# Kernel tuning notes

Hardware: AMD Instinct MI355X
Metric: run time of the kernel (lower is better)

The kernel has to match this reference:

```python
import jax, jax.numpy as jnp
import numpy as np

B, L, P, NH = 16384, 64, 2, 128
T = L // P          # number of patches (GRU steps)
NOUT = 1 << P       # softmax over 2**p possible patches


def setup_inputs() -> dict:
    key = jax.random.key(0)
    ks = jax.random.split(key, 10)
    s_in = 1.0 / np.sqrt(NH)
    x = jax.random.randint(ks[0], (B, L, 1), 0, 2).astype(jnp.float32)
    return {
        "x": x,
        # GRU params, torch layout: gates ordered (r, z, n)
        "w_ih": jax.random.normal(ks[1], (3 * NH, P), jnp.float32) * s_in,
        "w_hh": jax.random.normal(ks[2], (3 * NH, NH), jnp.float32) * s_in,
        "b_ih": jax.random.normal(ks[3], (3 * NH,), jnp.float32) * s_in,
        "b_hh": jax.random.normal(ks[4], (3 * NH,), jnp.float32) * s_in,
        # MLP head: Linear(Nh,Nh) -> ReLU -> Linear(Nh, 2**p) -> Softmax
        "w1": jax.random.normal(ks[5], (NH, NH), jnp.float32) * s_in,
        "b1": jax.random.normal(ks[6], (NH,), jnp.float32) * s_in,
        "w2": jax.random.normal(ks[7], (NOUT, NH), jnp.float32) * s_in,
        "b2": jax.random.normal(ks[8], (NOUT,), jnp.float32) * s_in,
    }


def _gru_mlp_logp(x, w_ih, w_hh, b_ih, b_hh, w1, b1, w2, b2):
    b = x.shape[0]
    patches = x.reshape(b, T, P)                       # Patch1D.forward
    # shift right by one patch (teacher forcing input), first step is zeros
    data = jnp.concatenate([jnp.zeros((b, 1, P), x.dtype), patches[:, :-1]], axis=1)
    # precompute all input-side gate projections: [B,T,3*Nh]
    xi = jnp.einsum('btp,gp->btg', data, w_ih) + b_ih

    def step(h, xi_t):
        gi_r, gi_z, gi_n = jnp.split(xi_t, 3, axis=-1)
        gh = h @ w_hh.T + b_hh
        gh_r, gh_z, gh_n = jnp.split(gh, 3, axis=-1)
        r = jax.nn.sigmoid(gi_r + gh_r)
        z = jax.nn.sigmoid(gi_z + gh_z)
        n = jnp.tanh(gi_n + r * gh_n)
        h_new = (1.0 - z) * n + z * h
        return h_new, h_new

    h0 = jnp.zeros((b, NH), x.dtype)
    _, hs = jax.lax.scan(step, h0, jnp.swapaxes(xi, 0, 1))  # [T,B,Nh]
    hs = jnp.swapaxes(hs, 0, 1)                              # [B,T,Nh]

    hid = jax.nn.relu(hs @ w1.T + b1)
    probs = jax.nn.softmax(hid @ w2.T + b2, axis=-1)         # [B,T,2**p]

    # genpatch2onehot: binary-encode each patch, little-endian (bit i -> 2**i)
    weights = (1 << jnp.arange(P)).astype(jnp.float32)
    idx = jnp.sum(patches * weights, axis=-1).astype(jnp.int32)  # [B,T]
    total = jnp.take_along_axis(probs, idx[..., None], axis=-1)[..., 0]
    return jnp.sum(jnp.log(total), axis=1)                   # [B]


def reference(x, w_ih, w_hh, b_ih, b_hh, w1, b1, w2, b2):
    return _gru_mlp_logp(x, w_ih, w_hh, b_ih, b_hh, w1, b1, w2, b2)
```

## Files before the change

kernel.cpp:

```cpp
#include <hip/hip_runtime.h>
#include <hip/hip_bf16.h>


#define NSTEP 32
#define BT    32
#define BLK   512

using s8v = __attribute__((ext_vector_type(8))) short;
using f4v = __attribute__((ext_vector_type(4))) float;

#define L2E 1.4426950408889634f
#define LN2 0.6931471805599453f

__device__ __forceinline__ unsigned short f2bf(float f) {
  __hip_bfloat16 h = __float2bfloat16(f);
  return __builtin_bit_cast(unsigned short, h);
}
__device__ __forceinline__ unsigned pkbf2(float a, float b) {
  return (unsigned)f2bf(a) | ((unsigned)f2bf(b) << 16);
}
__device__ __forceinline__ s8v pack8s(float sc, float4 u, float4 v) {
  s8v a;
  a[0]=(short)f2bf(sc*u.x); a[1]=(short)f2bf(sc*u.y); a[2]=(short)f2bf(sc*u.z); a[3]=(short)f2bf(sc*u.w);
  a[4]=(short)f2bf(sc*v.x); a[5]=(short)f2bf(sc*v.y); a[6]=(short)f2bf(sc*v.z); a[7]=(short)f2bf(sc*v.w);
  return a;
}
__device__ __forceinline__ f4v mfma16(s8v a, s8v b, f4v c) {
  return __builtin_amdgcn_mfma_f32_16x16x32_bf16(a, b, c, 0, 0, 0);
}
__device__ __forceinline__ float sigm2(float x) {
  return __builtin_amdgcn_rcpf(1.f + __builtin_amdgcn_exp2f(-x));
}
__device__ __forceinline__ float tanh2(float x) {
  return __builtin_fmaf(2.f, __builtin_amdgcn_rcpf(1.f + __builtin_amdgcn_exp2f(-x)), -1.f);
}

__global__ __launch_bounds__(BLK, 4) void prnn_kernel(
    const float* __restrict__ x, const float* __restrict__ w_ih,
    const float* __restrict__ w_hh, const float* __restrict__ b_ih,
    const float* __restrict__ b_hh, const float* __restrict__ w1,
    const float* __restrict__ b1, const float* __restrict__ w2,
    const float* __restrict__ b2, float* __restrict__ out) {

  __shared__ __align__(16) unsigned char lds_h[2][8192];
  __shared__ __align__(16) unsigned char lds_hid[2][8192];
  __shared__ __align__(16) unsigned char lds_wA1[8*4*64*16];
  __shared__ __align__(16) unsigned char lds_w2f[4*64*16];
  __shared__ __align__(16) float lds_xrz[64*4*4];
  __shared__ __align__(16) float lds_xn[32*4*4];
  __shared__ __align__(16) float lds_bb[256];
  __shared__ __align__(16) float lds_b2[4];
  __shared__ unsigned lds_idx[32*8];
  __shared__ float lds_lp[8][32];

  const int tid = threadIdx.x;
  const int bbase = blockIdx.x * BT;
  const int lane = tid & 63;
  const int lg = lane >> 4, ln = lane & 15;
  const int w = __builtin_amdgcn_readfirstlane(tid >> 6);

  if (tid < 256) {
    int b = tid >> 3, ch = tid & 7;
    const float* xp = x + (size_t)(bbase + b) * 64 + ch * 8;
    float4 v0 = *(const float4*)xp, v1 = *(const float4*)(xp + 4);
    unsigned pk = ((v0.x!=0.f?1u:0u) | (v0.y!=0.f?2u:0u))
               | (((v0.z!=0.f?1u:0u) | (v0.w!=0.f?2u:0u)) << 8)
               | (((v1.x!=0.f?1u:0u) | (v1.y!=0.f?2u:0u)) << 16)
               | (((v1.z!=0.f?1u:0u) | (v1.w!=0.f?2u:0u)) << 24);
    lds_idx[b*8 + ch] = pk;
  }
  if (tid < 256) {
    int j = tid;
    float base = b_ih[j] + b_hh[j];
    float wa = w_ih[2*j], wb = w_ih[2*j+1];
    int q = j >> 2, e = j & 3;
    #pragma unroll
    for (int v = 0; v < 4; ++v)
      lds_xrz[(q*4+v)*4 + e] = L2E * (base + ((v&1) ? wa : 0.f) + ((v&2) ? wb : 0.f));
  }
  if (tid < 128) {
    int j2 = 256 + tid;
    float bn = b_ih[j2];
    float wan = w_ih[2*j2], wbn = w_ih[2*j2+1];
    int qn = tid >> 2, en = tid & 3;
    #pragma unroll
    for (int v = 0; v < 4; ++v)
      lds_xn[(qn*4+v)*4 + en] = (2.f*L2E) * (bn + ((v&1) ? wan : 0.f) + ((v&2) ? wbn : 0.f));
  }
  if (tid < 128) lds_bb[tid] = (2.f*L2E) * b_hh[256 + tid];
  else if (tid < 256) lds_bb[tid] = b1[tid - 128];
  if (tid < 4) lds_b2[tid] = b2[tid];
  #pragma unroll
  for (int it = 0; it < 4; ++it) {
    int i = tid + it * BLK;
    int mt = i >> 8, ks = (i >> 6) & 3, l = i & 63;
    const float* src = w1 + (16*mt + (l & 15)) * 128 + ks*32 + (l >> 4)*8;
    *(s8v*)(lds_wA1 + ((mt*4 + ks)*64 + l)*16) = pack8s(1.f, *(const float4*)src, *(const float4*)(src+4));
  }
  if (tid < 256) {
    int ks = tid >> 6, l = tid & 63;
    s8v fr;
    #pragma unroll
    for (int e = 0; e < 8; ++e) fr[e] = (short)0;
    if ((l & 15) < 4) {
      const float* src = w2 + (l & 15) * 128 + ks*32 + (l >> 4)*8;
      fr = pack8s(1.f, *(const float4*)src, *(const float4*)(src + 4));
    }
    *(s8v*)(lds_w2f + (ks*64 + l)*16) = fr;
  }

  s8v Ar[4], Az[4], An[4];
  {
    const int row = 16*w + ln;
    #pragma unroll
    for (int ks = 0; ks < 4; ++ks) {
      const float* s0 = w_hh + row*128 + ks*32 + lg*8;
      Ar[ks] = pack8s(L2E, *(const float4*)s0, *(const float4*)(s0 + 4));
      const float* s1 = s0 + 128*128;
      Az[ks] = pack8s(L2E, *(const float4*)s1, *(const float4*)(s1 + 4));
      const float* s2 = s0 + 256*128;
      An[ks] = pack8s(2.f*L2E, *(const float4*)s2, *(const float4*)(s2 + 4));
    }
  }
  const int q = 4*w + lg;

  __syncthreads();

  unsigned pk0a=0, pk0b=0, pk1a=0, pk1b=0;
  #pragma unroll
  for (int w8 = 0; w8 < 4; ++w8) {
    unsigned u = lds_idx[ln*8 + w8];
    pk0a |= (((u&3u) | ((u>>6)&0xCu) | ((u>>12)&0x30u) | ((u>>18)&0xC0u)) << (8*w8));
    unsigned u2 = lds_idx[(16+ln)*8 + w8];
    pk1a |= (((u2&3u) | ((u2>>6)&0xCu) | ((u2>>12)&0x30u) | ((u2>>18)&0xC0u)) << (8*w8));
  }
  #pragma unroll
  for (int w8 = 4; w8 < 8; ++w8) {
    unsigned u = lds_idx[ln*8 + w8];
    pk0b |= (((u&3u) | ((u>>6)&0xCu) | ((u>>12)&0x30u) | ((u>>18)&0xC0u)) << (8*(w8-4)));
    unsigned u2 = lds_idx[(16+ln)*8 + w8];
    pk1b |= (((u2&3u) | ((u2>>6)&0xCu) | ((u2>>12)&0x30u) | ((u2>>18)&0xC0u)) << (8*(w8-4)));
  }

  const unsigned wroff = (unsigned)((((w>>1)*128) + 16*(2*(w&1) + (lg>>1)) + ln)*16 + 8*(lg&1));

  s8v Bf[4][2];
  #pragma unroll
  for (int ks = 0; ks < 4; ++ks)
    #pragma unroll
    for (int nt = 0; nt < 2; ++nt)
      #pragma unroll
      for (int e = 0; e < 8; ++e) Bf[ks][nt][e] = (short)0;
  f4v hfr[2];
  hfr[0][0]=0.f; hfr[0][1]=0.f; hfr[0][2]=0.f; hfr[0][3]=0.f;
  hfr[1] = hfr[0];
  float lp0 = 0.f, lp1 = 0.f;
  int pv0 = 0, pv1 = 0;

  auto do_p5 = [&](int u, int uslot) {
    const int ua = u & 7;
    const bool d0 = (w == ua), d1 = (w == (ua ^ 4));
    if (d0 | d1) {
      const int ntx = d1 ? 1 : 0;
      f4v la;
      if (lg == 0) la = *(const f4v*)lds_b2;
      else { la[0]=0.f; la[1]=0.f; la[2]=0.f; la[3]=0.f; }
      #pragma unroll
      for (int ks = 0; ks < 4; ++ks) {
        const s8v W2f = *(const s8v*)(lds_w2f + (ks*64 + lane)*16);
        const s8v Bh  = *(const s8v*)(&lds_hid[uslot][((ks*2 + ntx)*64 + lane)*16]);
        la = mfma16(W2f, Bh, la);
      }
      if (lg == 0) {
        const unsigned hsel = ntx ? ((u & 16) ? pk1b : pk1a) : ((u & 16) ? pk0b : pk0a);
        const int ic = (int)((hsel >> ((2*u) & 31)) & 3);
        float l0=la[0], l1=la[1], l2=la[2], l3=la[3];
        float m = fmaxf(fmaxf(l0, l1), fmaxf(l2, l3));
        float s = __builtin_amdgcn_exp2f((l0-m)*L2E) + __builtin_amdgcn_exp2f((l1-m)*L2E)
                + __builtin_amdgcn_exp2f((l2-m)*L2E) + __builtin_amdgcn_exp2f((l3-m)*L2E);
        float sel = (ic == 0) ? l0 : (ic == 1) ? l1 : (ic == 2) ? l2 : l3;
        float v = (sel - m) - __builtin_amdgcn_logf(s) * LN2;
        if (ntx) lp1 += v; else lp0 += v;
      }
    }
  };

  for (int tb = 0; tb < NSTEP; tb += 8) {
    #pragma unroll
    for (int k = 0; k < 8; ++k) {
      const int t = tb + k;
      const int slot = t & 1;
      #pragma unroll
      for (int nt = 0; nt < 2; ++nt) {
        const int var = nt ? pv1 : pv0;
        f4v aR = *(const f4v*)&lds_xrz[(q*4 + var)*4];
        f4v aZ = *(const f4v*)&lds_xrz[((q+32)*4 + var)*4];
        f4v aN = *(const f4v*)&lds_bb[q*4];
        #pragma unroll
        for (int ks = 0; ks < 4; ++ks) {
          aR = mfma16(Ar[ks], Bf[ks][nt], aR);
          aZ = mfma16(Az[ks], Bf[ks][nt], aZ);
          aN = mfma16(An[ks], Bf[ks][nt], aN);
        }
        const f4v xnv = *(const f4v*)&lds_xn[(q*4 + var)*4];
        f4v hn;
        #pragma unroll
        for (int r = 0; r < 4; ++r) {
          float R  = sigm2(aR[r]);
          float Z  = sigm2(aZ[r]);
          float Ng = tanh2(__builtin_fmaf(R, aN[r], xnv[r]));
          hn[r] = __builtin_fmaf(Z, hfr[nt][r] - Ng, Ng);
        }
        hfr[nt] = hn;
        uint2 wv;
        wv.x = pkbf2(hn[0], hn[1]);
        wv.y = pkbf2(hn[2], hn[3]);
        *(uint2*)(&lds_h[slot][wroff + (unsigned)(nt*1024)]) = wv;
      }
      __syncthreads();
      if (t > 0) do_p5(t - 1, slot ^ 1);
      #pragma unroll
      for (int ks = 0; ks < 4; ++ks)
        #pragma unroll
        for (int nt = 0; nt < 2; ++nt)
          Bf[ks][nt] = *(const s8v*)(&lds_h[slot][((ks*2 + nt)*64 + lane)*16]);
      const f4v b1i = *(const f4v*)&lds_bb[128 + q*4];
      f4v hc0 = b1i, hc1 = b1i;
      #pragma unroll
      for (int ks = 0; ks < 4; ++ks) {
        const s8v wf = *(const s8v*)(lds_wA1 + ((w*4 + ks)*64 + lane)*16);
        hc0 = mfma16(wf, Bf[ks][0], hc0);
        hc1 = mfma16(wf, Bf[ks][1], hc1);
      }
      {
        uint2 wv;
        wv.x = pkbf2(fmaxf(hc0[0],0.f), fmaxf(hc0[1],0.f));
        wv.y = pkbf2(fmaxf(hc0[2],0.f), fmaxf(hc0[3],0.f));
        *(uint2*)(&lds_hid[slot][wroff]) = wv;
        wv.x = pkbf2(fmaxf(hc1[0],0.f), fmaxf(hc1[1],0.f));
        wv.y = pkbf2(fmaxf(hc1[2],0.f), fmaxf(hc1[3],0.f));
        *(uint2*)(&lds_hid[slot][wroff + 1024u]) = wv;
      }
      {
        const unsigned g0 = (t & 16) ? pk0b : pk0a;
        const unsigned g1 = (t & 16) ? pk1b : pk1a;
        const int sh = (2*t) & 31;
        pv0 = (int)((g0 >> sh) & 3);
        pv1 = (int)((g1 >> sh) & 3);
      }
    }
  }

  __syncthreads();
  do_p5(NSTEP - 1, (NSTEP - 1) & 1);

  if (lg == 0) { lds_lp[w][ln] = lp0; lds_lp[w][16 + ln] = lp1; }
  __syncthreads();
  if (tid < 32) {
    float s = 0.f;
    #pragma unroll
    for (int ww = 0; ww < 8; ++ww) s += lds_lp[ww][tid];
    out[bbase + tid] = s;
  }
}

extern "C" void kernel_launch(void* const* d_in, const int* in_sizes, int n_in,
                              void* d_out, int out_size, void* d_ws, size_t ws_size,
                              hipStream_t stream) {
  const float* x    = (const float*)d_in[0];
  const float* w_ih = (const float*)d_in[1];
  const float* w_hh = (const float*)d_in[2];
  const float* b_ih = (const float*)d_in[3];
  const float* b_hh = (const float*)d_in[4];
  const float* w1   = (const float*)d_in[5];
  const float* b1   = (const float*)d_in[6];
  const float* w2   = (const float*)d_in[7];
  const float* b2   = (const float*)d_in[8];
  float* out = (float*)d_out;
  int B = in_sizes[0] / 64;
  int grid = B / BT;
  prnn_kernel<<<grid, BLK, 0, stream>>>(x, w_ih, w_hh, b_ih, b_hh, w1, b1, w2, b2, out);
}
```

Baseline: 111.2 us.

## Halve batch tile per block and preconvert MLP weights in a prep kernel

Each block now handles 16 sequences instead of 32, which doubles the grid and removes the second n-tile of work per wave. The w1/w2 bf16 fragments are built once by a separate prep kernel into workspace and read from global/L2 instead of being repacked into LDS per block. The head's softmax step is now done in-step behind an extra barrier rather than deferred, and LDS double-buffering is dropped. The trade is more barriers per step and global loads of weight fragments inside the recurrence loop, in exchange for more blocks and less LDS per block.

```diff
diff --git a/kernel.cpp b/kernel.cpp
--- a/kernel.cpp
+++ b/kernel.cpp
@@ -3,7 +3,7 @@
 
 
 #define NSTEP 32
-#define BT    32
+#define BT    16
 #define BLK   512
 
 using s8v = __attribute__((ext_vector_type(8))) short;
@@ -35,23 +35,42 @@
   return __builtin_fmaf(2.f, __builtin_amdgcn_rcpf(1.f + __builtin_amdgcn_exp2f(-x)), -1.f);
 }
 
+__global__ void prep_kernel(const float* __restrict__ w1, const float* __restrict__ w2,
+                            unsigned char* __restrict__ ws) {
+  const int task = blockIdx.x;
+  const int l = threadIdx.x;
+  if (task < 32) {
+    const int mt = task >> 2, ks = task & 3;
+    const float* src = w1 + (16*mt + (l & 15)) * 128 + ks*32 + (l >> 4)*8;
+    *(s8v*)(ws + (task*64 + l)*16) = pack8s(1.f, *(const float4*)src, *(const float4*)(src + 4));
+  } else {
+    const int ks = task - 32;
+    s8v fr;
+    #pragma unroll
+    for (int e = 0; e < 8; ++e) fr[e] = (short)0;
+    if ((l & 15) < 4) {
+      const float* src = w2 + (l & 15) * 128 + ks*32 + (l >> 4)*8;
+      fr = pack8s(1.f, *(const float4*)src, *(const float4*)(src + 4));
+    }
+    *(s8v*)(ws + 32768 + (ks*64 + l)*16) = fr;
+  }
+}
+
 __global__ __launch_bounds__(BLK, 4) void prnn_kernel(
     const float* __restrict__ x, const float* __restrict__ w_ih,
     const float* __restrict__ w_hh, const float* __restrict__ b_ih,
-    const float* __restrict__ b_hh, const float* __restrict__ w1,
-    const float* __restrict__ b1, const float* __restrict__ w2,
-    const float* __restrict__ b2, float* __restrict__ out) {
-
-  __shared__ __align__(16) unsigned char lds_h[2][8192];
-  __shared__ __align__(16) unsigned char lds_hid[2][8192];
-  __shared__ __align__(16) unsigned char lds_wA1[8*4*64*16];
-  __shared__ __align__(16) unsigned char lds_w2f[4*64*16];
+    const float* __restrict__ b_hh, const float* __restrict__ b1,
+    const float* __restrict__ b2, const unsigned char* __restrict__ ws,
+    float* __restrict__ out) {
+
+  __shared__ __align__(16) unsigned char lds_h[4*64*16];
+  __shared__ __align__(16) unsigned char lds_hid[4*64*16];
   __shared__ __align__(16) float lds_xrz[64*4*4];
   __shared__ __align__(16) float lds_xn[32*4*4];
   __shared__ __align__(16) float lds_bb[256];
   __shared__ __align__(16) float lds_b2[4];
-  __shared__ unsigned lds_idx[32*8];
-  __shared__ float lds_lp[8][32];
+  __shared__ unsigned lds_idx[16*8];
+  __shared__ float lds_lp[8][16];
 
   const int tid = threadIdx.x;
   const int bbase = blockIdx.x * BT;
@@ -59,7 +78,7 @@
   const int lg = lane >> 4, ln = lane & 15;
   const int w = __builtin_amdgcn_readfirstlane(tid >> 6);
 
-  if (tid < 256) {
+  if (tid < 128) {
     int b = tid >> 3, ch = tid & 7;
     const float* xp = x + (size_t)(bbase + b) * 64 + ch * 8;
     float4 v0 = *(const float4*)xp, v1 = *(const float4*)(xp + 4);
@@ -73,10 +92,10 @@
     int j = tid;
     float base = b_ih[j] + b_hh[j];
     float wa = w_ih[2*j], wb = w_ih[2*j+1];
-    int q = j >> 2, e = j & 3;
+    int qq = j >> 2, e = j & 3;
     #pragma unroll
     for (int v = 0; v < 4; ++v)
-      lds_xrz[(q*4+v)*4 + e] = L2E * (base + ((v&1) ? wa : 0.f) + ((v&2) ? wb : 0.f));
+      lds_xrz[(qq*4+v)*4 + e] = L2E * (base + ((v&1) ? wa : 0.f) + ((v&2) ? wb : 0.f));
   }
   if (tid < 128) {
     int j2 = 256 + tid;
@@ -90,24 +109,6 @@
   if (tid < 128) lds_bb[tid] = (2.f*L2E) * b_hh[256 + tid];
   else if (tid < 256) lds_bb[tid] = b1[tid - 128];
   if (tid < 4) lds_b2[tid] = b2[tid];
-  #pragma unroll
-  for (int it = 0; it < 4; ++it) {
-    int i = tid + it * BLK;
-    int mt = i >> 8, ks = (i >> 6) & 3, l = i & 63;
-    const float* src = w1 + (16*mt + (l & 15)) * 128 + ks*32 + (l >> 4)*8;
-    *(s8v*)(lds_wA1 + ((mt*4 + ks)*64 + l)*16) = pack8s(1.f, *(const float4*)src, *(const float4*)(src+4));
-  }
-  if (tid < 256) {
-    int ks = tid >> 6, l = tid & 63;
-    s8v fr;
-    #pragma unroll
-    for (int e = 0; e < 8; ++e) fr[e] = (short)0;
-    if ((l & 15) < 4) {
-      const float* src = w2 + (l & 15) * 128 + ks*32 + (l >> 4)*8;
-      fr = pack8s(1.f, *(const float4*)src, *(const float4*)(src + 4));
-    }
-    *(s8v*)(lds_w2f + (ks*64 + l)*16) = fr;
-  }
 
   s8v Ar[4], Az[4], An[4];
   {
@@ -123,84 +124,47 @@
     }
   }
   const int q = 4*w + lg;
+  const s8v* __restrict__ wsf = (const s8v*)ws;
 
   __syncthreads();
 
-  unsigned pk0a=0, pk0b=0, pk1a=0, pk1b=0;
+  unsigned pk0a = 0, pk0b = 0;
   #pragma unroll
   for (int w8 = 0; w8 < 4; ++w8) {
     unsigned u = lds_idx[ln*8 + w8];
     pk0a |= (((u&3u) | ((u>>6)&0xCu) | ((u>>12)&0x30u) | ((u>>18)&0xC0u)) << (8*w8));
-    unsigned u2 = lds_idx[(16+ln)*8 + w8];
-    pk1a |= (((u2&3u) | ((u2>>6)&0xCu) | ((u2>>12)&0x30u) | ((u2>>18)&0xC0u)) << (8*w8));
-  }
-  #pragma unroll
-  for (int w8 = 4; w8 < 8; ++w8) {
-    unsigned u = lds_idx[ln*8 + w8];
-    pk0b |= (((u&3u) | ((u>>6)&0xCu) | ((u>>12)&0x30u) | ((u>>18)&0xC0u)) << (8*(w8-4)));
-    unsigned u2 = lds_idx[(16+ln)*8 + w8];
-    pk1b |= (((u2&3u) | ((u2>>6)&0xCu) | ((u2>>12)&0x30u) | ((u2>>18)&0xC0u)) << (8*(w8-4)));
-  }
-
-  const unsigned wroff = (unsigned)((((w>>1)*128) + 16*(2*(w&1) + (lg>>1)) + ln)*16 + 8*(lg&1));
-
-  s8v Bf[4][2];
+    unsigned u2 = lds_idx[ln*8 + 4 + w8];
+    pk0b |= (((u2&3u) | ((u2>>6)&0xCu) | ((u2>>12)&0x30u) | ((u2>>18)&0xC0u)) << (8*w8));
+  }
+
+  const unsigned wroff =
+      (unsigned)((((w>>1)*64 + 16*(2*(w&1) + (lg>>1)) + ln)*16) + 8*(lg&1));
+
+  s8v Bf[4];
   #pragma unroll
   for (int ks = 0; ks < 4; ++ks)
     #pragma unroll
-    for (int nt = 0; nt < 2; ++nt)
-      #pragma unroll
-      for (int e = 0; e < 8; ++e) Bf[ks][nt][e] = (short)0;
-  f4v hfr[2];
-  hfr[0][0]=0.f; hfr[0][1]=0.f; hfr[0][2]=0.f; hfr[0][3]=0.f;
-  hfr[1] = hfr[0];
-  float lp0 = 0.f, lp1 = 0.f;
-  int pv0 = 0, pv1 = 0;
-
-  auto do_p5 = [&](int u, int uslot) {
-    const int ua = u & 7;
-    const bool d0 = (w == ua), d1 = (w == (ua ^ 4));
-    if (d0 | d1) {
-      const int ntx = d1 ? 1 : 0;
-      f4v la;
-      if (lg == 0) la = *(const f4v*)lds_b2;
-      else { la[0]=0.f; la[1]=0.f; la[2]=0.f; la[3]=0.f; }
-      #pragma unroll
-      for (int ks = 0; ks < 4; ++ks) {
-        const s8v W2f = *(const s8v*)(lds_w2f + (ks*64 + lane)*16);
-        const s8v Bh  = *(const s8v*)(&lds_hid[uslot][((ks*2 + ntx)*64 + lane)*16]);
-        la = mfma16(W2f, Bh, la);
-      }
-      if (lg == 0) {
-        const unsigned hsel = ntx ? ((u & 16) ? pk1b : pk1a) : ((u & 16) ? pk0b : pk0a);
-        const int ic = (int)((hsel >> ((2*u) & 31)) & 3);
-        float l0=la[0], l1=la[1], l2=la[2], l3=la[3];
-        float m = fmaxf(fmaxf(l0, l1), fmaxf(l2, l3));
-        float s = __builtin_amdgcn_exp2f((l0-m)*L2E) + __builtin_amdgcn_exp2f((l1-m)*L2E)
-                + __builtin_amdgcn_exp2f((l2-m)*L2E) + __builtin_amdgcn_exp2f((l3-m)*L2E);
-        float sel = (ic == 0) ? l0 : (ic == 1) ? l1 : (ic == 2) ? l2 : l3;
-        float v = (sel - m) - __builtin_amdgcn_logf(s) * LN2;
-        if (ntx) lp1 += v; else lp0 += v;
-      }
-    }
-  };
+    for (int e = 0; e < 8; ++e) Bf[ks][e] = (short)0;
+  f4v hfr;
+  hfr[0]=0.f; hfr[1]=0.f; hfr[2]=0.f; hfr[3]=0.f;
+  float lp0 = 0.f;
+  int pv0 = 0;
 
   for (int tb = 0; tb < NSTEP; tb += 8) {
+    const unsigned pc0 = (tb & 16) ? pk0b : pk0a;
     #pragma unroll
     for (int k = 0; k < 8; ++k) {
       const int t = tb + k;
-      const int slot = t & 1;
-      #pragma unroll
-      for (int nt = 0; nt < 2; ++nt) {
-        const int var = nt ? pv1 : pv0;
+      {
+        const int var = pv0;
         f4v aR = *(const f4v*)&lds_xrz[(q*4 + var)*4];
         f4v aZ = *(const f4v*)&lds_xrz[((q+32)*4 + var)*4];
         f4v aN = *(const f4v*)&lds_bb[q*4];
         #pragma unroll
         for (int ks = 0; ks < 4; ++ks) {
-          aR = mfma16(Ar[ks], Bf[ks][nt], aR);
-          aZ = mfma16(Az[ks], Bf[ks][nt], aZ);
-          aN = mfma16(An[ks], Bf[ks][nt], aN);
+          aR = mfma16(Ar[ks], Bf[ks], aR);
+          aZ = mfma16(Az[ks], Bf[ks], aZ);
+          aN = mfma16(An[ks], Bf[ks], aN);
         }
         const f4v xnv = *(const f4v*)&lds_xn[(q*4 + var)*4];
         f4v hn;
@@ -209,54 +173,55 @@
           float R  = sigm2(aR[r]);
           float Z  = sigm2(aZ[r]);
           float Ng = tanh2(__builtin_fmaf(R, aN[r], xnv[r]));
-          hn[r] = __builtin_fmaf(Z, hfr[nt][r] - Ng, Ng);
+          hn[r] = __builtin_fmaf(Z, hfr[r] - Ng, Ng);
         }
-        hfr[nt] = hn;
+        hfr = hn;
         uint2 wv;
         wv.x = pkbf2(hn[0], hn[1]);
         wv.y = pkbf2(hn[2], hn[3]);
-        *(uint2*)(&lds_h[slot][wroff + (unsigned)(nt*1024)]) = wv;
+        *(uint2*)(&lds_h[wroff]) = wv;
       }
       __syncthreads();
-      if (t > 0) do_p5(t - 1, slot ^ 1);
       #pragma unroll
       for (int ks = 0; ks < 4; ++ks)
-        #pragma unroll
-        for (int nt = 0; nt < 2; ++nt)
-          Bf[ks][nt] = *(const s8v*)(&lds_h[slot][((ks*2 + nt)*64 + lane)*16]);
-      const f4v b1i = *(const f4v*)&lds_bb[128 + q*4];
-      f4v hc0 = b1i, hc1 = b1i;
-      #pragma unroll
-      for (int ks = 0; ks < 4; ++ks) {
-        const s8v wf = *(const s8v*)(lds_wA1 + ((w*4 + ks)*64 + lane)*16);
-        hc0 = mfma16(wf, Bf[ks][0], hc0);
-        hc1 = mfma16(wf, Bf[ks][1], hc1);
+        Bf[ks] = *(const s8v*)(&lds_h[(ks*64 + lane)*16]);
+      {
+        f4v hc = *(const f4v*)&lds_bb[128 + q*4];
+        #pragma unroll
+        for (int ks = 0; ks < 4; ++ks)
+          hc = mfma16(wsf[(w*4 + ks)*64 + lane], Bf[ks], hc);
+        uint2 wv;
+        wv.x = pkbf2(fmaxf(hc[0],0.f), fmaxf(hc[1],0.f));
+        wv.y = pkbf2(fmaxf(hc[2],0.f), fmaxf(hc[3],0.f));
+        *(uint2*)(&lds_hid[wroff]) = wv;
       }
-      {
-        uint2 wv;
-        wv.x = pkbf2(fmaxf(hc0[0],0.f), fmaxf(hc0[1],0.f));
-        wv.y = pkbf2(fmaxf(hc0[2],0.f), fmaxf(hc0[3],0.f));
-        *(uint2*)(&lds_hid[slot][wroff]) = wv;
-        wv.x = pkbf2(fmaxf(hc1[0],0.f), fmaxf(hc1[1],0.f));
-        wv.y = pkbf2(fmaxf(hc1[2],0.f), fmaxf(hc1[3],0.f));
-        *(uint2*)(&lds_hid[slot][wroff + 1024u]) = wv;
+      __syncthreads();
+      const int ic0 = (int)((pc0 >> ((2*t) & 31)) & 3);
+      if (w == k) {
+        f4v la;
+        if (lg == 0) la = *(const f4v*)lds_b2;
+        else { la[0]=0.f; la[1]=0.f; la[2]=0.f; la[3]=0.f; }
+        #pragma unroll
+        for (int ks = 0; ks < 4; ++ks)
+          la = mfma16(wsf[2048 + ks*64 + lane],
+                      *(const s8v*)(&lds_hid[(ks*64 + lane)*16]), la);
+        if (lg == 0) {
+          const int ic = (int)(((t & 16) ? pk0b : pk0a) >> ((2*t) & 31)) & 3;
+          float l0=la[0], l1=la[1], l2=la[2], l3=la[3];
+          float m = fmaxf(fmaxf(l0, l1), fmaxf(l2, l3));
+          float s = __builtin_amdgcn_exp2f((l0-m)*L2E) + __builtin_amdgcn_exp2f((l1-m)*L2E)
+                  + __builtin_amdgcn_exp2f((l2-m)*L2E) + __builtin_amdgcn_exp2f((l3-m)*L2E);
+          float sel = (ic == 0) ? l0 : (ic == 1) ? l1 : (ic == 2) ? l2 : l3;
+          lp0 += (sel - m) - __builtin_amdgcn_logf(s) * LN2;
+        }
       }
-      {
-        const unsigned g0 = (t & 16) ? pk0b : pk0a;
-        const unsigned g1 = (t & 16) ? pk1b : pk1a;
-        const int sh = (2*t) & 31;
-        pv0 = (int)((g0 >> sh) & 3);
-        pv1 = (int)((g1 >> sh) & 3);
-      }
+      pv0 = ic0;
     }
   }
 
+  if (lg == 0) lds_lp[w][ln] = lp0;
   __syncthreads();
-  do_p5(NSTEP - 1, (NSTEP - 1) & 1);
-
-  if (lg == 0) { lds_lp[w][ln] = lp0; lds_lp[w][16 + ln] = lp1; }
-  __syncthreads();
-  if (tid < 32) {
+  if (tid < 16) {
     float s = 0.f;
     #pragma unroll
     for (int ww = 0; ww < 8; ++ww) s += lds_lp[ww][tid];
@@ -277,7 +242,11 @@
   const float* w2   = (const float*)d_in[7];
   const float* b2   = (const float*)d_in[8];
   float* out = (float*)d_out;
+  unsigned char* ws = (unsigned char*)d_ws;
+
+  prep_kernel<<<36, 64, 0, stream>>>(w1, w2, ws);
+
   int B = in_sizes[0] / 64;
   int grid = B / BT;
-  prnn_kernel<<<grid, BLK, 0, stream>>>(x, w_ih, w_hh, b_ih, b_hh, w1, b1, w2, b2, out);
-}
+  prnn_kernel<<<grid, BLK, 0, stream>>>(x, w_ih, w_hh, b_ih, b_hh, b1, b2, ws, out);
+}
```

Result: no change. 111.8 us (+0.6%).
